# Optimization experiments

Measured on AMD Instinct MI355X. Metric: run time of the kernel, lower is better.

The kernel has to match this reference:

```python
import jax, jax.numpy as jnp
import numpy as np

B, L = 32, 96
N = B * L
E = B * L * L
HID, LAT, EEMB = 128, 64, 32
NLAYERS = 3
LAMBDA_CONTRAST = 0.05


def _sinusoidal(t, dim):
    half = dim // 2
    freqs = jnp.exp(-jnp.log(10000.0) * jnp.arange(half, dtype=jnp.float32) / (half - 1))
    ang = t[:, None] * freqs[None, :]
    return jnp.concatenate([jnp.sin(ang), jnp.cos(ang)], axis=-1)


def _forward(H_0, X_0, H_1, X_1, cond_embedding, t_graph,
             Wi1, bi1, Wi2, bi2, Wi3, bi3, edge_table,
             We1, be1, We2, be2, Wx, Wh1, bh1, Wh2, bh2, Wout, bout,
             edges, chain_ids, generate_mask, lengths, shift):
    n = H_0.shape[0]
    b = lengths.shape[0]
    batch_ids = jnp.repeat(jnp.arange(b), lengths, total_repeat_length=n)
    t = t_graph[batch_ids]                      # (N,)
    mask = generate_mask
    mask_f = mask.astype(jnp.float32)

    # path interpolation
    tH = t[:, None]
    H_t = jnp.where(mask[:, None], (1.0 - tH) * H_0 + tH * H_1, H_1)
    X_t = jnp.where(mask[:, None], (1.0 - tH) * X_0 + tH * X_1, X_1)
    v_H_target = H_1 - H_0
    v_X_target = X_1 - X_0

    # edge types from chain-id masking (irregular gather)
    row, col = edges[0], edges[1]
    edge_types = (chain_ids[row] != chain_ids[col]).astype(jnp.int32)

    # --- velocity net ---
    t_embed = _sinusoidal(t, HID)
    h = jnp.concatenate([H_t, cond_embedding, t_embed], axis=-1)
    h = jax.nn.relu(h @ Wi1 + bi1)
    h = jax.nn.relu(h @ Wi2 + bi2)
    h = h @ Wi3 + bi3                            # (N, HID)
    eemb = edge_table[edge_types]                # (E, EEMB)

    X = X_t
    for l in range(NLAYERS):
        rel = X[row] - X[col]                    # (E, 3)
        d2 = jnp.sum(rel * rel, axis=-1, keepdims=True)
        ef = jnp.concatenate([h[row], h[col], d2, eemb], axis=-1)
        m = jax.nn.silu(ef @ We1[l] + be1[l])
        m = jax.nn.silu(m @ We2[l] + be2[l])     # (E, HID)
        coef = m @ Wx[l]                         # (E, 1)
        X = X + jax.ops.segment_sum(rel * coef, row, num_segments=n)
        agg = jax.ops.segment_sum(m, row, num_segments=n)
        hh = jnp.concatenate([h, agg], axis=-1)
        h = h + jax.nn.silu(hh @ Wh1[l] + bh1[l]) @ Wh2[l] + bh2[l]

    v_X_pred = jnp.where(mask[:, None], X, 0.0)
    v_H_pred = jnp.where(mask[:, None], h @ Wout + bout, 0.0)

    # --- losses ---
    msum = mask_f.sum() + 1e-8
    def masked_mse(pred, tgt):
        return (jnp.sum((pred - tgt) ** 2, axis=-1) * mask_f).sum() / msum
    loss_H_pos = masked_mse(v_H_pred, v_H_target)
    loss_X_pos = masked_mse(v_X_pred, v_X_target)

    # negatives: roll over node dim (matches torch indexing (arange+shift)%N)
    v_H_target_neg = jnp.roll(H_1, -shift, axis=0) - jnp.roll(H_0, -shift, axis=0)
    v_X_target_neg = jnp.roll(X_1, -shift, axis=0) - jnp.roll(X_0, -shift, axis=0)
    loss_H_neg = masked_mse(v_H_pred, v_H_target_neg)
    loss_X_neg = masked_mse(v_X_pred, v_X_target_neg)

    loss_H = loss_H_pos - LAMBDA_CONTRAST * loss_H_neg
    loss_X = loss_X_pos - LAMBDA_CONTRAST * loss_X_neg
    return jnp.stack([loss_H, loss_X, loss_H_pos, loss_X_pos, loss_H_neg, loss_X_neg])


def setup_inputs() -> dict:
    key = jax.random.key(0)
    ks = iter(jax.random.split(key, 40))
    def nrm(shape, fan_in):
        return jax.random.normal(next(ks), shape, dtype=jnp.float32) / np.sqrt(fan_in)

    # all-pairs edges within each graph (uniform lengths)
    idx = np.arange(L)
    rb, cb = np.repeat(idx, L), np.tile(idx, L)
    off = (np.arange(B) * L)[:, None]
    rows = (off + rb[None, :]).reshape(-1)
    cols = (off + cb[None, :]).reshape(-1)
    edges = jnp.asarray(np.stack([rows, cols]).astype(np.int32))

    d_in_mlp = LAT + 2 * HID       # 320
    d_in_e = 2 * HID + 1 + EEMB    # 289
    inp = {
        "H_0": jax.random.normal(next(ks), (N, LAT), dtype=jnp.float32),
        "X_0": jax.random.normal(next(ks), (N, 3), dtype=jnp.float32),
        "H_1": jax.random.normal(next(ks), (N, LAT), dtype=jnp.float32),
        "X_1": jax.random.normal(next(ks), (N, 3), dtype=jnp.float32),
        "cond_embedding": jax.random.normal(next(ks), (N, HID), dtype=jnp.float32),
        "t_graph": jax.random.uniform(next(ks), (B,), dtype=jnp.float32),
        "Wi1": nrm((d_in_mlp, HID), d_in_mlp), "bi1": jnp.zeros((HID,)),
        "Wi2": nrm((HID, HID), HID), "bi2": jnp.zeros((HID,)),
        "Wi3": nrm((HID, HID), HID), "bi3": jnp.zeros((HID,)),
        "edge_table": jax.random.normal(next(ks), (2, EEMB), dtype=jnp.float32),
        "We1": nrm((NLAYERS, d_in_e, HID), d_in_e), "be1": jnp.zeros((NLAYERS, HID)),
        "We2": nrm((NLAYERS, HID, HID), HID), "be2": jnp.zeros((NLAYERS, HID)),
        "Wx": nrm((NLAYERS, HID, 1), HID) * 0.01,
        "Wh1": nrm((NLAYERS, 2 * HID, HID), 2 * HID), "bh1": jnp.zeros((NLAYERS, HID)),
        "Wh2": nrm((NLAYERS, HID, HID), HID), "bh2": jnp.zeros((NLAYERS, HID)),
        "Wout": nrm((HID, LAT), HID), "bout": jnp.zeros((LAT,)),
        "edges": edges,
        "chain_ids": jax.random.randint(next(ks), (N,), 0, 3).astype(jnp.int32),
        "generate_mask": jax.random.bernoulli(next(ks), 0.5, (N,)),
        "lengths": jnp.full((B,), L, dtype=jnp.int32),
        "shift": 7,
    }
    return inp


def reference(H_0, X_0, H_1, X_1, cond_embedding, t_graph,
              Wi1, bi1, Wi2, bi2, Wi3, bi3, edge_table,
              We1, be1, We2, be2, Wx, Wh1, bh1, Wh2, bh2, Wout, bout,
              edges, chain_ids, generate_mask, lengths, shift):
    return _forward(H_0, X_0, H_1, X_1, cond_embedding, t_graph,
                    Wi1, bi1, Wi2, bi2, Wi3, bi3, edge_table,
                    We1, be1, We2, be2, Wx, Wh1, bh1, Wh2, bh2, Wout, bout,
                    edges, chain_ids, generate_mask, lengths, shift)
```

## Files before the change

### kernel.cpp

```cpp
#include <hip/hip_runtime.h>
#include <hip/hip_bf16.h>
#include <math.h>

#define NBATCH 32
#define LSEQ   96
#define NN     3072
#define HID    128
#define LAT    64
#define EEMB   32

#define OFF_H      0
#define OFF_X      (OFF_H   + NN*HID)
#define OFF_PA     (OFF_X   + NN*3)
#define OFF_AGG    (OFF_PA  + NN*HID)
#define OFF_DX     (OFF_AGG + NN*HID)
#define OFF_ET     (OFF_DX  + NN*3)
#define OFF_ACC    (OFF_ET  + 768)
#define OFF_NBID   (OFF_ACC + 8)
#define OFF_CUM    (OFF_NBID + NN)
#define OFF_PBH    (OFF_CUM + 40)
#define OFF_BPE    (OFF_PBH + NN*HID/2)
#define OFF_BAB    (OFF_BPE + 24576)
#define OFF_BH1    (OFF_BAB + 49152)
#define OFF_BH2    (OFF_BH1 + 49152)
#define OFF_BWO    (OFF_BH2 + 24576)
#define OFF_BWI1   (OFF_BWO + 4096)
#define OFF_BWI2   (OFF_BWI1 + 20480)
#define OFF_BWI3   (OFF_BWI2 + 8192)
#define OFF_CNT    (OFF_BWI3 + 8192)

typedef short bf16x8 __attribute__((ext_vector_type(8)));
typedef float f32x4  __attribute__((ext_vector_type(4)));

__device__ __forceinline__ short f2bf(float f) {
    unsigned u = __builtin_bit_cast(unsigned, f);
    unsigned r = (u + 0x7FFFu + ((u >> 16) & 1u)) >> 16;
    return (short)r;
}
__device__ __forceinline__ short2 f2bf2(float a, float b) {
    __hip_bfloat162 h = __float22bfloat162_rn(make_float2(a, b));
    short2 r;
    __builtin_memcpy(&r, &h, sizeof(r));
    return r;
}
__device__ __forceinline__ float bf2f(short s) {
    unsigned u = ((unsigned)(unsigned short)s) << 16;
    return __builtin_bit_cast(float, u);
}
__device__ __forceinline__ float silu(float z) {
    return z * __builtin_amdgcn_rcpf(1.0f + __expf(-z));
}

__global__ void k0_all(const float* __restrict__ edge_table, const float* __restrict__ We1,
                       const int* __restrict__ lengths, const float* __restrict__ We2,
                       const float* __restrict__ Wh1, const float* __restrict__ Wh2,
                       const float* __restrict__ Wout, const float* __restrict__ Wi1,
                       const float* __restrict__ Wi2, const float* __restrict__ Wi3,
                       float* __restrict__ ws) {
    int tid = threadIdx.x;
    if (blockIdx.x == 1472) {
        int* cum = (int*)(ws + OFF_CUM);
        int* nb  = (int*)(ws + OFF_NBID);
        float* et = ws + OFF_ET;
        if (tid == 0) {
            int s = 0;
            for (int b = 0; b < NBATCH; b++) { cum[b] = s; s += lengths[b]; }
            cum[NBATCH] = s;
        }
        if (tid < 8) ws[OFF_ACC + tid] = 0.0f;
        if (tid < 128) ((unsigned*)(ws + OFF_CNT))[tid] = 0u;
        __syncthreads();
        for (int i = tid; i < NN; i += blockDim.x) {
            int b = NBATCH - 1;
            for (int q = 0; q < NBATCH; q++) { if (i < cum[q + 1]) { b = q; break; } }
            nb[i] = b;
        }
        for (int idx = tid; idx < 3 * 2 * HID; idx += blockDim.x) {
            int c = idx & 127;
            int t = (idx >> 7) & 1;
            int l = idx >> 8;
            const float* w = We1 + (l * 289 + 257) * HID + c;
            const float* e = edge_table + t * EEMB;
            float s = 0.f;
            for (int k = 0; k < EEMB; k++) s += e[k] * w[k * HID];
            et[idx] = s;
        }
        return;
    }
    int idx = blockIdx.x * 256 + tid;
    short* bpe  = (short*)(ws + OFF_BPE);
    short* bab  = (short*)(ws + OFF_BAB);
    short* bh1  = (short*)(ws + OFF_BH1);
    short* bh2  = (short*)(ws + OFF_BH2);
    short* bwo  = (short*)(ws + OFF_BWO);
    short* bwi1 = (short*)(ws + OFF_BWI1);
    short* bwi2 = (short*)(ws + OFF_BWI2);
    short* bwi3 = (short*)(ws + OFF_BWI3);
    if (idx < 49152) {
        int k = idx & 127, n = (idx >> 7) & 127, l = idx >> 14;
        bpe[idx] = f2bf(We2[(l * 128 + k) * 128 + n]);
    } else if (idx < 147456) {
        int q = idx - 49152;
        int k = q & 127, n = (q >> 7) & 255, l = q >> 15;
        float v = (n < 128) ? We1[(l * 289 + k) * 128 + n]
                            : We1[(l * 289 + 128 + k) * 128 + (n - 128)];
        bab[q] = f2bf(v);
    } else if (idx < 245760) {
        int q = idx - 147456;
        int k = q & 255, n = (q >> 8) & 127, l = q >> 15;
        bh1[q] = f2bf(Wh1[(l * 256 + k) * 128 + n]);
    } else if (idx < 294912) {
        int q = idx - 245760;
        int k = q & 127, n = (q >> 7) & 127, l = q >> 14;
        bh2[q] = f2bf(Wh2[(l * 128 + k) * 128 + n]);
    } else if (idx < 303104) {
        int q = idx - 294912;
        int k = q & 127, n = q >> 7;
        bwo[q] = f2bf(Wout[k * 64 + n]);
    } else if (idx < 344064) {
        int q = idx - 303104;
        int n = q / 320, k = q - n * 320;
        bwi1[q] = f2bf(Wi1[k * 128 + n]);
    } else if (idx < 360448) {
        int q = idx - 344064;
        int k = q & 127, n = q >> 7;
        bwi2[q] = f2bf(Wi2[k * 128 + n]);
    } else if (idx < 376832) {
        int q = idx - 360448;
        int k = q & 127, n = q >> 7;
        bwi3[q] = f2bf(Wi3[k * 128 + n]);
    }
}

__global__ void __launch_bounds__(256)
k1s_node_init(const float* __restrict__ H0, const float* __restrict__ X0,
              const float* __restrict__ H1, const float* __restrict__ X1,
              const float* __restrict__ cond, const float* __restrict__ tg,
              const float* __restrict__ bi1, const float* __restrict__ bi2,
              const float* __restrict__ bi3, const float* __restrict__ be1,
              const int* __restrict__ gmask, float* __restrict__ ws) {
    __shared__ short u1[16 * 136];
    __shared__ short u2[16 * 136];
    int rowbase = blockIdx.x * 96 + blockIdx.y * 16;
    int tid = threadIdx.x;
    int w = tid >> 6, lane = tid & 63;
    int quad = lane >> 4, lp = lane & 15;
    int nodeA = rowbase + lp;
    const int* nb = (const int*)(ws + OFF_NBID);
    float t = tg[nb[nodeA]];
    float u = (gmask[nodeA] != 0) ? t : 1.0f;

    if (tid < 48) {
        int node = rowbase + tid / 3, d = tid % 3;
        float tn = tg[nb[node]];
        float un = (gmask[node] != 0) ? tn : 1.0f;
        ws[OFF_X + (size_t)node * 3 + d] =
            (1.0f - un) * X0[(size_t)node * 3 + d] + un * X1[(size_t)node * 3 + d];
    }

    const short* bwi1 = (const short*)(ws + OFF_BWI1);
    const short* bwi2 = (const short*)(ws + OFF_BWI2);
    const short* bwi3 = (const short*)(ws + OFF_BWI3);
    const short* bab  = (const short*)(ws + OFF_BAB);

    f32x4 acc[2];
    acc[0] = (f32x4){0.f, 0.f, 0.f, 0.f};
    acc[1] = (f32x4){0.f, 0.f, 0.f, 0.f};
    for (int s = 0; s < 10; s++) {
        int kb = s * 32 + quad * 8;
        float z[8];
        if (kb < 64) {
            const float* h0 = H0 + (size_t)nodeA * 64 + kb;
            const float* h1 = H1 + (size_t)nodeA * 64 + kb;
            #pragma unroll
            for (int e = 0; e < 8; e++) z[e] = (1.0f - u) * h0[e] + u * h1[e];
        } else if (kb < 192) {
            const float* cp = cond + (size_t)nodeA * 128 + (kb - 64);
            #pragma unroll
            for (int e = 0; e < 8; e++) z[e] = cp[e];
        } else if (kb < 256) {
            #pragma unroll
            for (int e = 0; e < 8; e++) {
                float c = (float)(kb - 192 + e);
                float fr = __expf(-9.2103403719761836f * c / 63.0f);
                z[e] = __sinf(t * fr);
            }
        } else {
            #pragma unroll
            for (int e = 0; e < 8; e++) {
                float c = (float)(kb - 256 + e);
                float fr = __expf(-9.2103403719761836f * c / 63.0f);
                z[e] = __cosf(t * fr);
            }
        }
        bf16x8 af;
        #pragma unroll
        for (int e = 0; e < 8; e += 2) {
            short2 p = f2bf2(z[e], z[e + 1]);
            af[e] = p.x; af[e + 1] = p.y;
        }
        #pragma unroll
        for (int i = 0; i < 2; i++) {
            int ct = 2 * w + i;
            bf16x8 bf = *(const bf16x8*)(bwi1 + (size_t)(16 * ct + lp) * 320 + kb);
            acc[i] = __builtin_amdgcn_mfma_f32_16x16x32_bf16(af, bf, acc[i], 0, 0, 0);
        }
    }
    #pragma unroll
    for (int i = 0; i < 2; i++) {
        int ch = 16 * (2 * w + i) + lp;
        float bb1 = bi1[ch];
        #pragma unroll
        for (int r = 0; r < 4; r++)
            u1[(quad * 4 + r) * 136 + ch] = f2bf(fmaxf(acc[i][r] + bb1, 0.0f));
    }
    __syncthreads();

    acc[0] = (f32x4){0.f, 0.f, 0.f, 0.f};
    acc[1] = (f32x4){0.f, 0.f, 0.f, 0.f};
    #pragma unroll
    for (int s = 0; s < 4; s++) {
        int kb = s * 32 + quad * 8;
        bf16x8 af = *(const bf16x8*)(u1 + lp * 136 + kb);
        #pragma unroll
        for (int i = 0; i < 2; i++) {
            int ct = 2 * w + i;
            bf16x8 bf = *(const bf16x8*)(bwi2 + (size_t)(16 * ct + lp) * 128 + kb);
            acc[i] = __builtin_amdgcn_mfma_f32_16x16x32_bf16(af, bf, acc[i], 0, 0, 0);
        }
    }
    #pragma unroll
    for (int i = 0; i < 2; i++) {
        int ch = 16 * (2 * w + i) + lp;
        float bb2 = bi2[ch];
        #pragma unroll
        for (int r = 0; r < 4; r++)
            u2[(quad * 4 + r) * 136 + ch] = f2bf(fmaxf(acc[i][r] + bb2, 0.0f));
    }
    __syncthreads();

    acc[0] = (f32x4){0.f, 0.f, 0.f, 0.f};
    acc[1] = (f32x4){0.f, 0.f, 0.f, 0.f};
    #pragma unroll
    for (int s = 0; s < 4; s++) {
        int kb = s * 32 + quad * 8;
        bf16x8 af = *(const bf16x8*)(u2 + lp * 136 + kb);
        #pragma unroll
        for (int i = 0; i < 2; i++) {
            int ct = 2 * w + i;
            bf16x8 bf = *(const bf16x8*)(bwi3 + (size_t)(16 * ct + lp) * 128 + kb);
            acc[i] = __builtin_amdgcn_mfma_f32_16x16x32_bf16(af, bf, acc[i], 0, 0, 0);
        }
    }
    #pragma unroll
    for (int i = 0; i < 2; i++) {
        int ch = 16 * (2 * w + i) + lp;
        float bb3 = bi3[ch];
        #pragma unroll
        for (int r = 0; r < 4; r++) {
            int row = quad * 4 + r;
            float h = acc[i][r] + bb3;
            ws[OFF_H + (size_t)(rowbase + row) * 128 + ch] = h;
            u1[row * 136 + ch] = f2bf(h);
        }
    }
    __syncthreads();

    f32x4 acc4[4];
    #pragma unroll
    for (int i = 0; i < 4; i++) acc4[i] = (f32x4){0.f, 0.f, 0.f, 0.f};
    #pragma unroll
    for (int s = 0; s < 4; s++) {
        int kb = s * 32 + quad * 8;
        bf16x8 af = *(const bf16x8*)(u1 + lp * 136 + kb);
        #pragma unroll
        for (int i = 0; i < 4; i++) {
            int ct4 = 4 * w + i;
            bf16x8 bf = *(const bf16x8*)(bab + (size_t)(16 * ct4 + lp) * 128 + kb);
            acc4[i] = __builtin_amdgcn_mfma_f32_16x16x32_bf16(af, bf, acc4[i], 0, 0, 0);
        }
    }
    short* pbh = (short*)(ws + OFF_PBH);
    #pragma unroll
    for (int i = 0; i < 4; i++) {
        int ct4 = 4 * w + i;
        #pragma unroll
        for (int r = 0; r < 4; r++) {
            int node = rowbase + quad * 4 + r;
            if (ct4 < 8) {
                int ch = 16 * ct4 + lp;
                ws[OFF_PA + (size_t)node * 128 + ch] = acc4[i][r] + be1[ch];
            } else {
                int ch = 16 * (ct4 - 8) + lp;
                pbh[(size_t)node * 128 + ch] = f2bf(acc4[i][r]);
            }
        }
    }
}

#define KG 4
#define SMC_BS    0
#define SMC_AGG   32768
#define SMC_PE0   35840
#define SMC_PE1   37888
#define SMC_WC    39936
#define SMC_COEF  40448
#define SMC_XT    40832
#define SMC_CI    40880
__global__ void __launch_bounds__(384)
k3v_edge(const float* __restrict__ We1, const float* __restrict__ Wx,
         const float* __restrict__ be2, const int* __restrict__ chain,
         int l, float* __restrict__ ws) {
    __shared__ __align__(16) char smem[40896];
    short* bS    = (short*)(smem + SMC_BS);
    float* aggP  = (float*)(smem + SMC_AGG);
    float* pe0S  = (float*)(smem + SMC_PE0);
    float* pe1S  = (float*)(smem + SMC_PE1);
    float* wcS   = (float*)(smem + SMC_WC);
    float* coefS = (float*)(smem + SMC_COEF);
    float* xT    = (float*)(smem + SMC_XT);
    int*   ciS   = (int*)  (smem + SMC_CI);

    int tid = threadIdx.x;
    int i0 = blockIdx.x * KG;
    int colbase = (i0 / 96) * 96;
    const float* Xc = ws + OFF_X;

    {
        const short* bpe = (const short*)(ws + OFF_BPE) + (size_t)l * 128 * 128;
        for (int idx = tid; idx < 2048; idx += 384) {
            int t = idx >> 8, s = (idx >> 6) & 3, ln = idx & 63;
            int lq = ln >> 4, lpp = ln & 15;
            *(bf16x8*)(bS + idx * 8) =
                *(const bf16x8*)(bpe + (size_t)(16 * t + lpp) * 128 + s * 32 + lq * 8);
        }
        if (tid < 128) {
            float et0 = ws[OFF_ET + l * 256 + tid];
            float et1 = ws[OFF_ET + l * 256 + 128 + tid];
            #pragma unroll
            for (int g = 0; g < KG; g++) {
                float pav = ws[OFF_PA + (size_t)(i0 + g) * 128 + tid];
                pe0S[g * 128 + tid] = pav + et0;
                pe1S[g * 128 + tid] = pav + et1;
            }
            wcS[tid] = We1[(l * 289 + 256) * 128 + tid];
        }
        if (tid < KG * 3) xT[tid] = Xc[(size_t)(i0 + tid / 3) * 3 + tid % 3];
        if (tid < KG) ciS[tid] = chain[i0 + tid];
    }

    int w = tid >> 6, lane = tid & 63;
    int quad = lane >> 4, lp = lane & 15;
    int jA = 16 * w + lp;
    const short* pbrow = (const short*)(ws + OFF_PBH) + (size_t)(colbase + jA) * 128;
    bf16x8 pbv[4];
    #pragma unroll
    for (int s = 0; s < 4; s++) pbv[s] = *(const bf16x8*)(pbrow + s * 32 + quad * 8);
    float xr0 = Xc[(size_t)(colbase + jA) * 3 + 0];
    float xr1 = Xc[(size_t)(colbase + jA) * 3 + 1];
    float xr2 = Xc[(size_t)(colbase + jA) * 3 + 2];
    int cj = chain[colbase + jA];
    float be2r[8], wxr[8];
    #pragma unroll
    for (int t = 0; t < 8; t++) {
        int ch = 16 * t + lp;
        be2r[t] = be2[l * 128 + ch];
        wxr[t]  = Wx[l * 128 + ch];
    }
    float ex0 = 0.f, ex1 = 0.f;
    if (w < 3) {
        ex0 = Xc[(size_t)(colbase + lane) * 3 + w];
        if (lane < 32) ex1 = Xc[(size_t)(colbase + lane + 64) * 3 + w];
    }
    __syncthreads();

    #pragma unroll
    for (int g = 0; g < KG; g++) {
        float rx = xT[g * 3 + 0] - xr0;
        float ry = xT[g * 3 + 1] - xr1;
        float rz = xT[g * 3 + 2] - xr2;
        float d2j = rx * rx + ry * ry + rz * rz;
        const float* peB = ((cj != ciS[g]) ? pe1S : pe0S) + g * 128;

        f32x4 acc[8];
        #pragma unroll
        for (int t = 0; t < 8; t++) acc[t] = (f32x4){0.f, 0.f, 0.f, 0.f};

        #pragma unroll
        for (int s = 0; s < 4; s++) {
            int kb = s * 32 + quad * 8;
            float4 p0 = *(const float4*)(peB + kb);
            float4 p1 = *(const float4*)(peB + kb + 4);
            float4 w0 = *(const float4*)(wcS + kb);
            float4 w1 = *(const float4*)(wcS + kb + 4);
            float pe[8] = {p0.x, p0.y, p0.z, p0.w, p1.x, p1.y, p1.z, p1.w};
            float wc[8] = {w0.x, w0.y, w0.z, w0.w, w1.x, w1.y, w1.z, w1.w};
            float z[8];
            #pragma unroll
            for (int e = 0; e < 8; e++)
                z[e] = silu(pe[e] + bf2f(pbv[s][e]) + d2j * wc[e]);
            bf16x8 af;
            #pragma unroll
            for (int e = 0; e < 8; e += 2) {
                short2 p = f2bf2(z[e], z[e + 1]);
                af[e] = p.x; af[e + 1] = p.y;
            }
            #pragma unroll
            for (int t = 0; t < 8; t++) {
                bf16x8 bf = *(const bf16x8*)(bS + ((t * 4 + s) * 64 + lane) * 8);
                acc[t] = __builtin_amdgcn_mfma_f32_16x16x32_bf16(af, bf, acc[t], 0, 0, 0);
            }
        }

        float cp[4] = {0.f, 0.f, 0.f, 0.f};
        #pragma unroll
        for (int t = 0; t < 8; t++) {
            float ag = 0.f;
            #pragma unroll
            for (int r = 0; r < 4; r++) {
                float m2 = silu(acc[t][r] + be2r[t]);
                ag += m2;
                cp[r] += m2 * wxr[t];
            }
            ag += __shfl_xor(ag, 16);
            ag += __shfl_xor(ag, 32);
            if (lane < 16) aggP[w * 128 + 16 * t + lp] = ag;
        }
        #pragma unroll
        for (int r = 0; r < 4; r++) {
            float v = cp[r];
            v += __shfl_xor(v, 1);
            v += __shfl_xor(v, 2);
            v += __shfl_xor(v, 4);
            v += __shfl_xor(v, 8);
            if (lp == 0) coefS[16 * w + quad * 4 + r] = v;
        }
        __syncthreads();

        if (tid < 128) {
            float s = 0.f;
            #pragma unroll
            for (int q = 0; q < 6; q++) s += aggP[q * 128 + tid];
            ws[OFF_AGG + (size_t)(i0 + g) * 128 + tid] = s;
        }
        if (w < 3) {
            float v = (xT[g * 3 + w] - ex0) * coefS[lane];
            if (lane < 32) v += (xT[g * 3 + w] - ex1) * coefS[lane + 64];
            #pragma unroll
            for (int o = 32; o > 0; o >>= 1) v += __shfl_down(v, o);
            if (lane == 0) ws[OFF_DX + (size_t)(i0 + g) * 3 + w] = v;
        }
        __syncthreads();
    }
}

__global__ void __launch_bounds__(256)
k4s_node_post(const float* __restrict__ bh1, const float* __restrict__ bh2,
              const float* __restrict__ be1, const float* __restrict__ bout,
              const float* __restrict__ H0, const float* __restrict__ X0,
              const float* __restrict__ H1, const float* __restrict__ X1,
              const int* __restrict__ gmask, const int* __restrict__ shiftp,
              int l, float* __restrict__ ws, float* __restrict__ out) {
    __shared__ short uS[16 * 136];
    __shared__ short hS[16 * 136];
    __shared__ float redE[4], redN[4];
    __shared__ float sxp, sxn, scnt;
    int rowbase = blockIdx.x * 96 + blockIdx.y * 16;
    int tid = threadIdx.x;
    int w = tid >> 6, lane = tid & 63;
    int quad = lane >> 4, lp = lane & 15;
    int nodeA = rowbase + lp;
    const short* b1 = (const short*)(ws + OFF_BH1) + (size_t)l * 128 * 256;
    const short* b2 = (const short*)(ws + OFF_BH2) + (size_t)l * 128 * 128;

    if (tid == 0) { sxp = 0.f; sxn = 0.f; scnt = 0.f; }
    if (tid < 48) {
        int node = rowbase + tid / 3, d = tid % 3;
        ws[OFF_X + (size_t)node * 3 + d] += ws[OFF_DX + (size_t)node * 3 + d];
    }

    f32x4 acc[2];
    acc[0] = (f32x4){0.f, 0.f, 0.f, 0.f};
    acc[1] = (f32x4){0.f, 0.f, 0.f, 0.f};
    #pragma unroll
    for (int s = 0; s < 8; s++) {
        int kb = s * 32 + quad * 8;
        const float* src = (kb < 128) ? (ws + OFF_H + (size_t)nodeA * 128 + kb)
                                      : (ws + OFF_AGG + (size_t)nodeA * 128 + (kb - 128));
        bf16x8 af;
        #pragma unroll
        for (int e = 0; e < 8; e += 2) {
            short2 p = f2bf2(src[e], src[e + 1]);
            af[e] = p.x; af[e + 1] = p.y;
        }
        #pragma unroll
        for (int i = 0; i < 2; i++) {
            int ct = 2 * w + i;
            bf16x8 bf = *(const bf16x8*)(b1 + (size_t)(16 * ct + lp) * 256 + kb);
            acc[i] = __builtin_amdgcn_mfma_f32_16x16x32_bf16(af, bf, acc[i], 0, 0, 0);
        }
    }
    #pragma unroll
    for (int i = 0; i < 2; i++) {
        int ch = 16 * (2 * w + i) + lp;
        float bb1 = bh1[l * 128 + ch];
        #pragma unroll
        for (int r = 0; r < 4; r++)
            uS[(quad * 4 + r) * 136 + ch] = f2bf(silu(acc[i][r] + bb1));
    }
    __syncthreads();

    acc[0] = (f32x4){0.f, 0.f, 0.f, 0.f};
    acc[1] = (f32x4){0.f, 0.f, 0.f, 0.f};
    #pragma unroll
    for (int s = 0; s < 4; s++) {
        int kb = s * 32 + quad * 8;
        bf16x8 af = *(const bf16x8*)(uS + lp * 136 + kb);
        #pragma unroll
        for (int i = 0; i < 2; i++) {
            int ct = 2 * w + i;
            bf16x8 bf = *(const bf16x8*)(b2 + (size_t)(16 * ct + lp) * 128 + kb);
            acc[i] = __builtin_amdgcn_mfma_f32_16x16x32_bf16(af, bf, acc[i], 0, 0, 0);
        }
    }
    #pragma unroll
    for (int i = 0; i < 2; i++) {
        int ch = 16 * (2 * w + i) + lp;
        float bb2 = bh2[l * 128 + ch];
        #pragma unroll
        for (int r = 0; r < 4; r++) {
            int row = quad * 4 + r;
            size_t off = OFF_H + (size_t)(rowbase + row) * 128 + ch;
            float h = ws[off] + acc[i][r] + bb2;
            ws[off] = h;
            hS[row * 136 + ch] = f2bf(h);
        }
    }
    __syncthreads();

    if (l < 2) {
        const short* bab = (const short*)(ws + OFF_BAB) + (size_t)(l + 1) * 256 * 128;
        f32x4 acc4[4];
        #pragma unroll
        for (int i = 0; i < 4; i++) acc4[i] = (f32x4){0.f, 0.f, 0.f, 0.f};
        #pragma unroll
        for (int s = 0; s < 4; s++) {
            int kb = s * 32 + quad * 8;
            bf16x8 af = *(const bf16x8*)(hS + lp * 136 + kb);
            #pragma unroll
            for (int i = 0; i < 4; i++) {
                int ct4 = 4 * w + i;
                bf16x8 bf = *(const bf16x8*)(bab + (size_t)(16 * ct4 + lp) * 128 + kb);
                acc4[i] = __builtin_amdgcn_mfma_f32_16x16x32_bf16(af, bf, acc4[i], 0, 0, 0);
            }
        }
        short* pbh = (short*)(ws + OFF_PBH);
        #pragma unroll
        for (int i = 0; i < 4; i++) {
            int ct4 = 4 * w + i;
            #pragma unroll
            for (int r = 0; r < 4; r++) {
                int node = rowbase + quad * 4 + r;
                if (ct4 < 8) {
                    int ch = 16 * ct4 + lp;
                    ws[OFF_PA + (size_t)node * 128 + ch] = acc4[i][r] + be1[(l + 1) * 128 + ch];
                } else {
                    int ch = 16 * (ct4 - 8) + lp;
                    pbh[(size_t)node * 128 + ch] = f2bf(acc4[i][r]);
                }
            }
        }
    } else {
        const short* bwo = (const short*)(ws + OFF_BWO);
        f32x4 accv = (f32x4){0.f, 0.f, 0.f, 0.f};
        #pragma unroll
        for (int s = 0; s < 4; s++) {
            int kb = s * 32 + quad * 8;
            bf16x8 af = *(const bf16x8*)(hS + lp * 136 + kb);
            bf16x8 bf = *(const bf16x8*)(bwo + (size_t)(16 * w + lp) * 128 + kb);
            accv = __builtin_amdgcn_mfma_f32_16x16x32_bf16(af, bf, accv, 0, 0, 0);
        }
        int s = shiftp[0] % NN; if (s < 0) s += NN;
        int col = 16 * w + lp;
        float bo = bout[col];
        float ep = 0.f, en = 0.f;
        #pragma unroll
        for (int r = 0; r < 4; r++) {
            int row = rowbase + quad * 4 + r;
            if (gmask[row] != 0) {
                int ip = row + s; if (ip >= NN) ip -= NN;
                float v  = accv[r] + bo;
                float tp = H1[(size_t)row * 64 + col] - H0[(size_t)row * 64 + col];
                float tn = H1[(size_t)ip * 64 + col]  - H0[(size_t)ip * 64 + col];
                float dp = v - tp, dn = v - tn;
                ep += dp * dp;
                en += dn * dn;
            }
        }
        #pragma unroll
        for (int o = 1; o < 64; o <<= 1) {
            ep += __shfl_xor(ep, o);
            en += __shfl_xor(en, o);
        }
        if (lane == 0) { redE[w] = ep; redN[w] = en; }

        if (tid < 16) {
            int node = rowbase + tid;
            if (gmask[node] != 0) {
                int ip = node + s; if (ip >= NN) ip -= NN;
                float xp = 0.f, xn = 0.f;
                #pragma unroll
                for (int d = 0; d < 3; d++) {
                    float xv  = ws[OFF_X + (size_t)node * 3 + d];
                    float tpx = X1[(size_t)node * 3 + d] - X0[(size_t)node * 3 + d];
                    float tnx = X1[(size_t)ip * 3 + d]   - X0[(size_t)ip * 3 + d];
                    xp += (xv - tpx) * (xv - tpx);
                    xn += (xv - tnx) * (xv - tnx);
                }
                atomicAdd(&sxp, xp);
                atomicAdd(&sxn, xn);
                atomicAdd(&scnt, 1.0f);
            }
        }
        __syncthreads();
        if (tid == 0) {
            float eT = redE[0] + redE[1] + redE[2] + redE[3];
            float nT = redN[0] + redN[1] + redN[2] + redN[3];
            float* acc0 = ws + OFF_ACC;
            atomicAdd(acc0 + 0, eT);
            atomicAdd(acc0 + 2, nT);
            atomicAdd(acc0 + 1, sxp);
            atomicAdd(acc0 + 3, sxn);
            atomicAdd(acc0 + 4, scnt);
            __threadfence();
            unsigned o2 = atomicAdd((unsigned*)(ws + OFF_CNT) + 96, 1u);
            if (o2 == 191u) {
                __threadfence();
                float a0 = atomicAdd(acc0 + 0, 0.0f);
                float a1 = atomicAdd(acc0 + 1, 0.0f);
                float a2 = atomicAdd(acc0 + 2, 0.0f);
                float a3 = atomicAdd(acc0 + 3, 0.0f);
                float a4 = atomicAdd(acc0 + 4, 0.0f);
                float msum = a4 + 1e-8f;
                float lhp = a0 / msum, lxp = a1 / msum;
                float lhn = a2 / msum, lxn = a3 / msum;
                out[0] = lhp - 0.05f * lhn;
                out[1] = lxp - 0.05f * lxn;
                out[2] = lhp;
                out[3] = lxp;
                out[4] = lhn;
                out[5] = lxn;
            }
        }
    }
}

extern "C" void kernel_launch(void* const* d_in, const int* in_sizes, int n_in,
                              void* d_out, int out_size, void* d_ws, size_t ws_size,
                              hipStream_t stream) {
    (void)in_sizes; (void)n_in; (void)out_size; (void)ws_size;
    const float* H0   = (const float*)d_in[0];
    const float* X0   = (const float*)d_in[1];
    const float* H1   = (const float*)d_in[2];
    const float* X1   = (const float*)d_in[3];
    const float* cond = (const float*)d_in[4];
    const float* tg   = (const float*)d_in[5];
    const float* Wi1  = (const float*)d_in[6];
    const float* bi1  = (const float*)d_in[7];
    const float* Wi2  = (const float*)d_in[8];
    const float* bi2  = (const float*)d_in[9];
    const float* Wi3  = (const float*)d_in[10];
    const float* bi3  = (const float*)d_in[11];
    const float* etab = (const float*)d_in[12];
    const float* We1  = (const float*)d_in[13];
    const float* be1  = (const float*)d_in[14];
    const float* We2  = (const float*)d_in[15];
    const float* be2  = (const float*)d_in[16];
    const float* Wx   = (const float*)d_in[17];
    const float* Wh1  = (const float*)d_in[18];
    const float* bh1  = (const float*)d_in[19];
    const float* Wh2  = (const float*)d_in[20];
    const float* bh2  = (const float*)d_in[21];
    const float* Wout = (const float*)d_in[22];
    const float* bout = (const float*)d_in[23];
    const int* chain   = (const int*)d_in[25];
    const int* gmask   = (const int*)d_in[26];
    const int* lengths = (const int*)d_in[27];
    const int* shiftp  = (const int*)d_in[28];
    float* ws  = (float*)d_ws;
    float* out = (float*)d_out;

    k0_all<<<1473, 256, 0, stream>>>(etab, We1, lengths, We2, Wh1, Wh2,
                                     Wout, Wi1, Wi2, Wi3, ws);
    k1s_node_init<<<dim3(NBATCH, 6), 256, 0, stream>>>(H0, X0, H1, X1, cond, tg,
                                                       bi1, bi2, bi3, be1, gmask, ws);
    for (int l = 0; l < 3; l++) {
        k3v_edge<<<NN / KG, 384, 0, stream>>>(We1, Wx, be2, chain, l, ws);
        k4s_node_post<<<dim3(NBATCH, 6), 256, 0, stream>>>(bh1, bh2, be1, bout,
                                                           H0, X0, H1, X1, gmask, shiftp,
                                                           l, ws, out);
    }
}
```

Baseline: 376.2 us.

## Process two target nodes per pass in edge kernel, reusing B fragments

Restructures the edge-message kernel so each pass handles two target nodes at once. Each B-matrix fragment loaded from shared memory now feeds two MFMAs, and half of the block barriers go away because aggregation and coefficient buffers are double-sized per node. It also moves be2/Wx into shared memory, stops keeping the pb row in registers across the loop, and adds a minimum-occupancy hint of 5 blocks. In exchange it uses more shared memory and more live accumulator and A-fragment registers, which could limit occupancy or cause spills.

```diff
diff --git a/kernel.cpp b/kernel.cpp
--- a/kernel.cpp
+++ b/kernel.cpp
@@ -301,22 +301,26 @@
 #define KG 4
 #define SMC_BS    0
 #define SMC_AGG   32768
-#define SMC_PE0   35840
-#define SMC_PE1   37888
-#define SMC_WC    39936
-#define SMC_COEF  40448
-#define SMC_XT    40832
-#define SMC_CI    40880
-__global__ void __launch_bounds__(384)
+#define SMC_PE0   45056
+#define SMC_PE1   47104
+#define SMC_WC    49152
+#define SMC_BE2   49664
+#define SMC_WX    50176
+#define SMC_COEF  50688
+#define SMC_XT    52224
+#define SMC_CI    52272
+__global__ void __launch_bounds__(384, 5)
 k3v_edge(const float* __restrict__ We1, const float* __restrict__ Wx,
          const float* __restrict__ be2, const int* __restrict__ chain,
          int l, float* __restrict__ ws) {
-    __shared__ __align__(16) char smem[40896];
+    __shared__ __align__(16) char smem[52288];
     short* bS    = (short*)(smem + SMC_BS);
     float* aggP  = (float*)(smem + SMC_AGG);
     float* pe0S  = (float*)(smem + SMC_PE0);
     float* pe1S  = (float*)(smem + SMC_PE1);
     float* wcS   = (float*)(smem + SMC_WC);
+    float* be2S  = (float*)(smem + SMC_BE2);
+    float* wxS   = (float*)(smem + SMC_WX);
     float* coefS = (float*)(smem + SMC_COEF);
     float* xT    = (float*)(smem + SMC_XT);
     int*   ciS   = (int*)  (smem + SMC_CI);
@@ -343,7 +347,9 @@
                 pe0S[g * 128 + tid] = pav + et0;
                 pe1S[g * 128 + tid] = pav + et1;
             }
-            wcS[tid] = We1[(l * 289 + 256) * 128 + tid];
+            wcS[tid]  = We1[(l * 289 + 256) * 128 + tid];
+            be2S[tid] = be2[l * 128 + tid];
+            wxS[tid]  = Wx[l * 128 + tid];
         }
         if (tid < KG * 3) xT[tid] = Xc[(size_t)(i0 + tid / 3) * 3 + tid % 3];
         if (tid < KG) ciS[tid] = chain[i0 + tid];
@@ -353,20 +359,10 @@
     int quad = lane >> 4, lp = lane & 15;
     int jA = 16 * w + lp;
     const short* pbrow = (const short*)(ws + OFF_PBH) + (size_t)(colbase + jA) * 128;
-    bf16x8 pbv[4];
-    #pragma unroll
-    for (int s = 0; s < 4; s++) pbv[s] = *(const bf16x8*)(pbrow + s * 32 + quad * 8);
     float xr0 = Xc[(size_t)(colbase + jA) * 3 + 0];
     float xr1 = Xc[(size_t)(colbase + jA) * 3 + 1];
     float xr2 = Xc[(size_t)(colbase + jA) * 3 + 2];
     int cj = chain[colbase + jA];
-    float be2r[8], wxr[8];
-    #pragma unroll
-    for (int t = 0; t < 8; t++) {
-        int ch = 16 * t + lp;
-        be2r[t] = be2[l * 128 + ch];
-        wxr[t]  = Wx[l * 128 + ch];
-    }
     float ex0 = 0.f, ex1 = 0.f;
     if (w < 3) {
         ex0 = Xc[(size_t)(colbase + lane) * 3 + w];
@@ -375,82 +371,108 @@
     __syncthreads();
 
     #pragma unroll
-    for (int g = 0; g < KG; g++) {
-        float rx = xT[g * 3 + 0] - xr0;
-        float ry = xT[g * 3 + 1] - xr1;
-        float rz = xT[g * 3 + 2] - xr2;
-        float d2j = rx * rx + ry * ry + rz * rz;
-        const float* peB = ((cj != ciS[g]) ? pe1S : pe0S) + g * 128;
-
-        f32x4 acc[8];
-        #pragma unroll
-        for (int t = 0; t < 8; t++) acc[t] = (f32x4){0.f, 0.f, 0.f, 0.f};
-
+    for (int gr = 0; gr < 2; gr++) {
+        int g0 = 2 * gr, g1 = 2 * gr + 1;
+        float rx0 = xT[g0 * 3 + 0] - xr0, ry0 = xT[g0 * 3 + 1] - xr1, rz0 = xT[g0 * 3 + 2] - xr2;
+        float rx1 = xT[g1 * 3 + 0] - xr0, ry1 = xT[g1 * 3 + 1] - xr1, rz1 = xT[g1 * 3 + 2] - xr2;
+        float d20 = rx0 * rx0 + ry0 * ry0 + rz0 * rz0;
+        float d21 = rx1 * rx1 + ry1 * ry1 + rz1 * rz1;
+        const float* peB0 = ((cj != ciS[g0]) ? pe1S : pe0S) + g0 * 128;
+        const float* peB1 = ((cj != ciS[g1]) ? pe1S : pe0S) + g1 * 128;
+
+        bf16x8 af0[4], af1[4];
         #pragma unroll
         for (int s = 0; s < 4; s++) {
             int kb = s * 32 + quad * 8;
-            float4 p0 = *(const float4*)(peB + kb);
-            float4 p1 = *(const float4*)(peB + kb + 4);
+            bf16x8 pb = *(const bf16x8*)(pbrow + kb);
             float4 w0 = *(const float4*)(wcS + kb);
             float4 w1 = *(const float4*)(wcS + kb + 4);
-            float pe[8] = {p0.x, p0.y, p0.z, p0.w, p1.x, p1.y, p1.z, p1.w};
-            float wc[8] = {w0.x, w0.y, w0.z, w0.w, w1.x, w1.y, w1.z, w1.w};
-            float z[8];
-            #pragma unroll
-            for (int e = 0; e < 8; e++)
-                z[e] = silu(pe[e] + bf2f(pbv[s][e]) + d2j * wc[e]);
-            bf16x8 af;
+            float wcv[8] = {w0.x, w0.y, w0.z, w0.w, w1.x, w1.y, w1.z, w1.w};
+            float4 pa0 = *(const float4*)(peB0 + kb);
+            float4 pa1 = *(const float4*)(peB0 + kb + 4);
+            float4 pb0 = *(const float4*)(peB1 + kb);
+            float4 pb1 = *(const float4*)(peB1 + kb + 4);
+            float pe0v[8] = {pa0.x, pa0.y, pa0.z, pa0.w, pa1.x, pa1.y, pa1.z, pa1.w};
+            float pe1v[8] = {pb0.x, pb0.y, pb0.z, pb0.w, pb1.x, pb1.y, pb1.z, pb1.w};
+            float z0[8], z1[8];
+            #pragma unroll
+            for (int e = 0; e < 8; e++) {
+                float pbf = bf2f(pb[e]);
+                z0[e] = silu(pe0v[e] + pbf + d20 * wcv[e]);
+                z1[e] = silu(pe1v[e] + pbf + d21 * wcv[e]);
+            }
             #pragma unroll
             for (int e = 0; e < 8; e += 2) {
-                short2 p = f2bf2(z[e], z[e + 1]);
-                af[e] = p.x; af[e + 1] = p.y;
-            }
-            #pragma unroll
-            for (int t = 0; t < 8; t++) {
+                short2 p0 = f2bf2(z0[e], z0[e + 1]);
+                short2 p1 = f2bf2(z1[e], z1[e + 1]);
+                af0[s][e] = p0.x; af0[s][e + 1] = p0.y;
+                af1[s][e] = p1.x; af1[s][e + 1] = p1.y;
+            }
+        }
+
+        float cp0[4] = {0.f, 0.f, 0.f, 0.f};
+        float cp1[4] = {0.f, 0.f, 0.f, 0.f};
+        #pragma unroll
+        for (int t = 0; t < 8; t++) {
+            f32x4 a0 = (f32x4){0.f, 0.f, 0.f, 0.f};
+            f32x4 a1 = (f32x4){0.f, 0.f, 0.f, 0.f};
+            #pragma unroll
+            for (int s = 0; s < 4; s++) {
                 bf16x8 bf = *(const bf16x8*)(bS + ((t * 4 + s) * 64 + lane) * 8);
-                acc[t] = __builtin_amdgcn_mfma_f32_16x16x32_bf16(af, bf, acc[t], 0, 0, 0);
-            }
-        }
-
-        float cp[4] = {0.f, 0.f, 0.f, 0.f};
-        #pragma unroll
-        for (int t = 0; t < 8; t++) {
-            float ag = 0.f;
+                a0 = __builtin_amdgcn_mfma_f32_16x16x32_bf16(af0[s], bf, a0, 0, 0, 0);
+                a1 = __builtin_amdgcn_mfma_f32_16x16x32_bf16(af1[s], bf, a1, 0, 0, 0);
+            }
+            float be2v = be2S[16 * t + lp];
+            float wxv  = wxS[16 * t + lp];
+            float ag0 = 0.f, ag1 = 0.f;
             #pragma unroll
             for (int r = 0; r < 4; r++) {
-                float m2 = silu(acc[t][r] + be2r[t]);
-                ag += m2;
-                cp[r] += m2 * wxr[t];
-            }
-            ag += __shfl_xor(ag, 16);
-            ag += __shfl_xor(ag, 32);
-            if (lane < 16) aggP[w * 128 + 16 * t + lp] = ag;
+                float m20 = silu(a0[r] + be2v);
+                float m21 = silu(a1[r] + be2v);
+                ag0 += m20; ag1 += m21;
+                cp0[r] += m20 * wxv;
+                cp1[r] += m21 * wxv;
+            }
+            ag0 += __shfl_xor(ag0, 16); ag0 += __shfl_xor(ag0, 32);
+            ag1 += __shfl_xor(ag1, 16); ag1 += __shfl_xor(ag1, 32);
+            if (lane < 16) {
+                aggP[(g0 * 6 + w) * 128 + 16 * t + lp] = ag0;
+                aggP[(g1 * 6 + w) * 128 + 16 * t + lp] = ag1;
+            }
         }
         #pragma unroll
         for (int r = 0; r < 4; r++) {
-            float v = cp[r];
-            v += __shfl_xor(v, 1);
-            v += __shfl_xor(v, 2);
-            v += __shfl_xor(v, 4);
-            v += __shfl_xor(v, 8);
-            if (lp == 0) coefS[16 * w + quad * 4 + r] = v;
+            float v0 = cp0[r], v1 = cp1[r];
+            v0 += __shfl_xor(v0, 1); v1 += __shfl_xor(v1, 1);
+            v0 += __shfl_xor(v0, 2); v1 += __shfl_xor(v1, 2);
+            v0 += __shfl_xor(v0, 4); v1 += __shfl_xor(v1, 4);
+            v0 += __shfl_xor(v0, 8); v1 += __shfl_xor(v1, 8);
+            if (lp == 0) {
+                coefS[g0 * 96 + 16 * w + quad * 4 + r] = v0;
+                coefS[g1 * 96 + 16 * w + quad * 4 + r] = v1;
+            }
         }
         __syncthreads();
 
-        if (tid < 128) {
+        if (tid < 256) {
+            int gg = tid >> 7, ch = tid & 127;
+            int g = 2 * gr + gg;
             float s = 0.f;
             #pragma unroll
-            for (int q = 0; q < 6; q++) s += aggP[q * 128 + tid];
-            ws[OFF_AGG + (size_t)(i0 + g) * 128 + tid] = s;
+            for (int q = 0; q < 6; q++) s += aggP[(g * 6 + q) * 128 + ch];
+            ws[OFF_AGG + (size_t)(i0 + g) * 128 + ch] = s;
         }
         if (w < 3) {
-            float v = (xT[g * 3 + w] - ex0) * coefS[lane];
-            if (lane < 32) v += (xT[g * 3 + w] - ex1) * coefS[lane + 64];
-            #pragma unroll
-            for (int o = 32; o > 0; o >>= 1) v += __shfl_down(v, o);
-            if (lane == 0) ws[OFF_DX + (size_t)(i0 + g) * 3 + w] = v;
-        }
-        __syncthreads();
+            #pragma unroll
+            for (int gg = 0; gg < 2; gg++) {
+                int g = 2 * gr + gg;
+                float v = (xT[g * 3 + w] - ex0) * coefS[g * 96 + lane];
+                if (lane < 32) v += (xT[g * 3 + w] - ex1) * coefS[g * 96 + lane + 64];
+                #pragma unroll
+                for (int o = 32; o > 0; o >>= 1) v += __shfl_down(v, o);
+                if (lane == 0) ws[OFF_DX + (size_t)(i0 + g) * 3 + w] = v;
+            }
+        }
     }
 }
 
```

Result: slower. 513.4 us (+36.5%).

## Remap edge kernel so each wave owns one source node over all columns

Applied to the files above, without the earlier changes.

The edge kernel now gives each of six waves one source node and loops it over all 96 column nodes in 16-wide tiles. Before, all waves split the columns of each node and combined partial sums through shared memory with two block barriers per node. Aggregation and coordinate updates are now accumulated in registers and reduced with wave shuffles, removing the per-node barriers and the shared-memory reduction. Column features, coordinates and chain ids are staged in LDS, which grows shared memory to about 67KB and may reduce occupancy. More MFMA work is issued per wave, with the A fragments built once per tile.

```diff
diff --git a/kernel.cpp b/kernel.cpp
--- a/kernel.cpp
+++ b/kernel.cpp
@@ -298,28 +298,26 @@
     }
 }
 
-#define KG 4
-#define SMC_BS    0
-#define SMC_AGG   32768
-#define SMC_PE0   35840
-#define SMC_PE1   37888
-#define SMC_WC    39936
-#define SMC_COEF  40448
-#define SMC_XT    40832
-#define SMC_CI    40880
+#define KG 6
+#define S_BS    0
+#define S_PB    32768
+#define S_PE0   58880
+#define S_PE1   61952
+#define S_WC    65024
+#define S_XC    65536
+#define S_CH    66688
 __global__ void __launch_bounds__(384)
-k3v_edge(const float* __restrict__ We1, const float* __restrict__ Wx,
+k3w_edge(const float* __restrict__ We1, const float* __restrict__ Wx,
          const float* __restrict__ be2, const int* __restrict__ chain,
          int l, float* __restrict__ ws) {
-    __shared__ __align__(16) char smem[40896];
-    short* bS    = (short*)(smem + SMC_BS);
-    float* aggP  = (float*)(smem + SMC_AGG);
-    float* pe0S  = (float*)(smem + SMC_PE0);
-    float* pe1S  = (float*)(smem + SMC_PE1);
-    float* wcS   = (float*)(smem + SMC_WC);
-    float* coefS = (float*)(smem + SMC_COEF);
-    float* xT    = (float*)(smem + SMC_XT);
-    int*   ciS   = (int*)  (smem + SMC_CI);
+    __shared__ __align__(16) char smem[67072];
+    short* bS    = (short*)(smem + S_BS);
+    short* pbS   = (short*)(smem + S_PB);
+    float* pe0S  = (float*)(smem + S_PE0);
+    float* pe1S  = (float*)(smem + S_PE1);
+    float* wcS   = (float*)(smem + S_WC);
+    float* xcS   = (float*)(smem + S_XC);
+    int*   chS   = (int*)  (smem + S_CH);
 
     int tid = threadIdx.x;
     int i0 = blockIdx.x * KG;
@@ -334,6 +332,12 @@
             *(bf16x8*)(bS + idx * 8) =
                 *(const bf16x8*)(bpe + (size_t)(16 * t + lpp) * 128 + s * 32 + lq * 8);
         }
+        const short* pbh = (const short*)(ws + OFF_PBH);
+        for (int idx = tid; idx < 1536; idx += 384) {
+            int j = idx >> 4, kc = (idx & 15) * 8;
+            *(bf16x8*)(pbS + j * 136 + kc) =
+                *(const bf16x8*)(pbh + (size_t)(colbase + j) * 128 + kc);
+        }
         if (tid < 128) {
             float et0 = ws[OFF_ET + l * 256 + tid];
             float et1 = ws[OFF_ET + l * 256 + 128 + tid];
@@ -345,21 +349,12 @@
             }
             wcS[tid] = We1[(l * 289 + 256) * 128 + tid];
         }
-        if (tid < KG * 3) xT[tid] = Xc[(size_t)(i0 + tid / 3) * 3 + tid % 3];
-        if (tid < KG) ciS[tid] = chain[i0 + tid];
+        if (tid < 288) xcS[tid] = Xc[(size_t)colbase * 3 + tid];
+        if (tid < 96)  chS[tid] = chain[colbase + tid];
     }
 
     int w = tid >> 6, lane = tid & 63;
     int quad = lane >> 4, lp = lane & 15;
-    int jA = 16 * w + lp;
-    const short* pbrow = (const short*)(ws + OFF_PBH) + (size_t)(colbase + jA) * 128;
-    bf16x8 pbv[4];
-    #pragma unroll
-    for (int s = 0; s < 4; s++) pbv[s] = *(const bf16x8*)(pbrow + s * 32 + quad * 8);
-    float xr0 = Xc[(size_t)(colbase + jA) * 3 + 0];
-    float xr1 = Xc[(size_t)(colbase + jA) * 3 + 1];
-    float xr2 = Xc[(size_t)(colbase + jA) * 3 + 2];
-    int cj = chain[colbase + jA];
     float be2r[8], wxr[8];
     #pragma unroll
     for (int t = 0; t < 8; t++) {
@@ -367,48 +362,60 @@
         be2r[t] = be2[l * 128 + ch];
         wxr[t]  = Wx[l * 128 + ch];
     }
-    float ex0 = 0.f, ex1 = 0.f;
-    if (w < 3) {
-        ex0 = Xc[(size_t)(colbase + lane) * 3 + w];
-        if (lane < 32) ex1 = Xc[(size_t)(colbase + lane + 64) * 3 + w];
-    }
     __syncthreads();
 
-    #pragma unroll
-    for (int g = 0; g < KG; g++) {
-        float rx = xT[g * 3 + 0] - xr0;
-        float ry = xT[g * 3 + 1] - xr1;
-        float rz = xT[g * 3 + 2] - xr2;
-        float d2j = rx * rx + ry * ry + rz * rz;
-        const float* peB = ((cj != ciS[g]) ? pe1S : pe0S) + g * 128;
-
-        f32x4 acc[8];
-        #pragma unroll
-        for (int t = 0; t < 8; t++) acc[t] = (f32x4){0.f, 0.f, 0.f, 0.f};
-
+    int g  = i0 + w;
+    int gl = (i0 - colbase) + w;
+    float xg0 = xcS[gl * 3 + 0], xg1 = xcS[gl * 3 + 1], xg2 = xcS[gl * 3 + 2];
+    int cig = chS[gl];
+    const float* pe0w = pe0S + w * 128;
+    const float* pe1w = pe1S + w * 128;
+
+    float agReg[8];
+    #pragma unroll
+    for (int t = 0; t < 8; t++) agReg[t] = 0.f;
+    float dxa0 = 0.f, dxa1 = 0.f, dxa2 = 0.f;
+
+    #pragma unroll
+    for (int f = 0; f < 6; f++) {
+        int j = 16 * f + lp;
+        float dx = xg0 - xcS[j * 3 + 0];
+        float dy = xg1 - xcS[j * 3 + 1];
+        float dz = xg2 - xcS[j * 3 + 2];
+        float d2 = dx * dx + dy * dy + dz * dz;
+        const float* peB = (chS[j] != cig) ? pe1w : pe0w;
+
+        bf16x8 af[4];
         #pragma unroll
         for (int s = 0; s < 4; s++) {
             int kb = s * 32 + quad * 8;
+            bf16x8 pb = *(const bf16x8*)(pbS + j * 136 + kb);
+            float4 w0 = *(const float4*)(wcS + kb);
+            float4 w1 = *(const float4*)(wcS + kb + 4);
+            float wcv[8] = {w0.x, w0.y, w0.z, w0.w, w1.x, w1.y, w1.z, w1.w};
             float4 p0 = *(const float4*)(peB + kb);
             float4 p1 = *(const float4*)(peB + kb + 4);
-            float4 w0 = *(const float4*)(wcS + kb);
-            float4 w1 = *(const float4*)(wcS + kb + 4);
-            float pe[8] = {p0.x, p0.y, p0.z, p0.w, p1.x, p1.y, p1.z, p1.w};
-            float wc[8] = {w0.x, w0.y, w0.z, w0.w, w1.x, w1.y, w1.z, w1.w};
+            float pev[8] = {p0.x, p0.y, p0.z, p0.w, p1.x, p1.y, p1.z, p1.w};
             float z[8];
             #pragma unroll
             for (int e = 0; e < 8; e++)
-                z[e] = silu(pe[e] + bf2f(pbv[s][e]) + d2j * wc[e]);
-            bf16x8 af;
+                z[e] = silu(pev[e] + bf2f(pb[e]) + d2 * wcv[e]);
             #pragma unroll
             for (int e = 0; e < 8; e += 2) {
                 short2 p = f2bf2(z[e], z[e + 1]);
-                af[e] = p.x; af[e + 1] = p.y;
-            }
-            #pragma unroll
-            for (int t = 0; t < 8; t++) {
+                af[s][e] = p.x; af[s][e + 1] = p.y;
+            }
+        }
+
+        f32x4 acc[8];
+        #pragma unroll
+        for (int t = 0; t < 8; t++) acc[t] = (f32x4){0.f, 0.f, 0.f, 0.f};
+        #pragma unroll
+        for (int t = 0; t < 8; t++) {
+            #pragma unroll
+            for (int s = 0; s < 4; s++) {
                 bf16x8 bf = *(const bf16x8*)(bS + ((t * 4 + s) * 64 + lane) * 8);
-                acc[t] = __builtin_amdgcn_mfma_f32_16x16x32_bf16(af, bf, acc[t], 0, 0, 0);
+                acc[t] = __builtin_amdgcn_mfma_f32_16x16x32_bf16(af[s], bf, acc[t], 0, 0, 0);
             }
         }
 
@@ -424,7 +431,7 @@
             }
             ag += __shfl_xor(ag, 16);
             ag += __shfl_xor(ag, 32);
-            if (lane < 16) aggP[w * 128 + 16 * t + lp] = ag;
+            agReg[t] += ag;
         }
         #pragma unroll
         for (int r = 0; r < 4; r++) {
@@ -433,24 +440,27 @@
             v += __shfl_xor(v, 2);
             v += __shfl_xor(v, 4);
             v += __shfl_xor(v, 8);
-            if (lp == 0) coefS[16 * w + quad * 4 + r] = v;
-        }
-        __syncthreads();
-
-        if (tid < 128) {
-            float s = 0.f;
-            #pragma unroll
-            for (int q = 0; q < 6; q++) s += aggP[q * 128 + tid];
-            ws[OFF_AGG + (size_t)(i0 + g) * 128 + tid] = s;
-        }
-        if (w < 3) {
-            float v = (xT[g * 3 + w] - ex0) * coefS[lane];
-            if (lane < 32) v += (xT[g * 3 + w] - ex1) * coefS[lane + 64];
-            #pragma unroll
-            for (int o = 32; o > 0; o >>= 1) v += __shfl_down(v, o);
-            if (lane == 0) ws[OFF_DX + (size_t)(i0 + g) * 3 + w] = v;
-        }
-        __syncthreads();
+            if (lp == 0) {
+                int jj = 16 * f + quad * 4 + r;
+                dxa0 += (xg0 - xcS[jj * 3 + 0]) * v;
+                dxa1 += (xg1 - xcS[jj * 3 + 1]) * v;
+                dxa2 += (xg2 - xcS[jj * 3 + 2]) * v;
+            }
+        }
+    }
+
+    if (lane < 16) {
+        #pragma unroll
+        for (int t = 0; t < 8; t++)
+            ws[OFF_AGG + (size_t)g * 128 + 16 * t + lane] = agReg[t];
+    }
+    dxa0 += __shfl_xor(dxa0, 16); dxa0 += __shfl_xor(dxa0, 32);
+    dxa1 += __shfl_xor(dxa1, 16); dxa1 += __shfl_xor(dxa1, 32);
+    dxa2 += __shfl_xor(dxa2, 16); dxa2 += __shfl_xor(dxa2, 32);
+    if (lane == 0) {
+        ws[OFF_DX + (size_t)g * 3 + 0] = dxa0;
+        ws[OFF_DX + (size_t)g * 3 + 1] = dxa1;
+        ws[OFF_DX + (size_t)g * 3 + 2] = dxa2;
     }
 }
 
@@ -695,7 +705,7 @@
     k1s_node_init<<<dim3(NBATCH, 6), 256, 0, stream>>>(H0, X0, H1, X1, cond, tg,
                                                        bi1, bi2, bi3, be1, gmask, ws);
     for (int l = 0; l < 3; l++) {
-        k3v_edge<<<NN / KG, 384, 0, stream>>>(We1, Wx, be2, chain, l, ws);
+        k3w_edge<<<NN / KG, 384, 0, stream>>>(We1, Wx, be2, chain, l, ws);
         k4s_node_post<<<dim3(NBATCH, 6), 256, 0, stream>>>(bh1, bh2, be1, bout,
                                                            H0, X0, H1, X1, gmask, shiftp,
                                                            l, ws, out);
```

New measurement: 356.8 us. -5.2%, faster.
